# Performance work log

Hardware: AMD Instinct MI355X
Metric: run time of the kernel (lower is better)

## Reference

```python
import jax, jax.numpy as jnp
import numpy as np

B, W, H = 16384, 16, 16
NUM_CLASSES = 1024
EMBED = 4
OUT = 1024

def setup_inputs() -> dict:
    key = jax.random.key(0)
    k0, k1, k2 = jax.random.split(key, 3)
    x = jax.random.randint(k0, (B, W, H), 0, NUM_CLASSES, dtype=jnp.int32)
    W_embed = jax.random.normal(k1, (NUM_CLASSES, EMBED), dtype=jnp.float32) * 0.02
    b_embed = jnp.zeros((EMBED,), dtype=jnp.float32)
    W_dense = jax.random.normal(k2, (EMBED * W * H, OUT), dtype=jnp.float32) * 0.02
    b_dense = jnp.zeros((OUT,), dtype=jnp.float32)
    return {"x": x, "W_embed": W_embed, "b_embed": b_embed, "W_dense": W_dense, "b_dense": b_dense}

def reference(x, W_embed, b_embed, W_dense, b_dense):
    # one_hot(x, C) @ W_embed + b_embed is mathematically a row-gather of W_embed
    emb = W_embed[x] + b_embed                 # (B, W, H, EMBED)
    flat = emb.reshape(emb.shape[0], -1)        # (B, W*H*EMBED)  == rearrange '... w h c -> ... (w h c)'
    return flat @ W_dense + b_dense             # (B, OUT)
```

## Files before the change

kernel.cpp:

```cpp
#include <hip/hip_runtime.h>
#include <stdint.h>
#include <stddef.h>

typedef __attribute__((ext_vector_type(8))) short bf16x8;
typedef __attribute__((ext_vector_type(4))) short bf16x4;
typedef __attribute__((ext_vector_type(4))) float f32x4;

typedef const __attribute__((address_space(1))) void* gptr1_t;
typedef __attribute__((address_space(3))) void* lptr3_t;

#define GLOAD_LDS16(gp, lp) \
  __builtin_amdgcn_global_load_lds((gptr1_t)(gp), (lptr3_t)(lp), 16, 0, 0)

__device__ __forceinline__ uint16_t f2bf(float f) {
  uint32_t u = __builtin_bit_cast(uint32_t, f);
  u += 0x7fffu + ((u >> 16) & 1u);
  return (uint16_t)(u >> 16);
}

#define MB   16384
#define NP   256
#define KDIM 1024
#define NDIM 1024
#define NCLS 1024

#define BM  128
#define BN  256
#define BK  64
#define NK  (KDIM / BK)


__global__ void build_bt_kernel(const float* __restrict__ Wd,
                                uint16_t* __restrict__ Btf) {
  __shared__ uint16_t tile[32][33];
  const int k0 = blockIdx.y * 32;
  const int n0 = blockIdx.x * 32;
  const int tx = threadIdx.x;
  const int ty = threadIdx.y;
  #pragma unroll
  for (int r = 0; r < 32; r += 8)
    tile[ty + r][tx] = f2bf(Wd[(size_t)(k0 + ty + r) * NDIM + n0 + tx]);
  __syncthreads();
  #pragma unroll
  for (int r = 0; r < 32; r += 8) {
    const int n = n0 + ty + r;
    const int k = k0 + tx;
    const int bn = n >> 8, g = (n >> 4) & 15, m = n & 15;
    const int kt = k >> 6, h = (k >> 5) & 1, q = (k >> 3) & 3, e = k & 7;
    Btf[(size_t)((bn * 16 + kt) * 2 + h) * 8192 + (size_t)(g * 64 + q * 16 + m) * 8 + e]
        = tile[tx][ty + r];
  }
}

__global__ __launch_bounds__(512) void fused_gemm_kernel(
    const int* __restrict__ x,
    const float* __restrict__ We,
    const float* __restrict__ be,
    const uint16_t* __restrict__ Btf,
    const float* __restrict__ bias,
    float* __restrict__ C) {
  __shared__ __align__(16) uint16_t web[NCLS * 4];
  __shared__ __align__(16) uint16_t As[2 * 4096];
  __shared__ __align__(16) uint16_t Bs[2 * 8192];

  const int tid  = threadIdx.x;
  const int bm   = blockIdx.x;
  const int bn   = blockIdx.y;
  const int w    = tid >> 6;
  const int l    = tid & 63;
  const int wr   = w >> 2;
  const int wc   = w & 3;
  const int lm   = l & 15;
  const int q4   = l >> 4;

  const int row0 = bm * BM;
  const int col0 = bn * BN;

  {
    const float4 bb = *(const float4*)be;
    #pragma unroll
    for (int c0 = 0; c0 < NCLS; c0 += 512) {
      const int c = c0 + tid;
      const float4 wv = *(const float4*)(We + (size_t)c * 4);
      bf16x4 t;
      t[0] = (short)f2bf(wv.x + bb.x);
      t[1] = (short)f2bf(wv.y + bb.y);
      t[2] = (short)f2bf(wv.z + bb.z);
      t[3] = (short)f2bf(wv.w + bb.w);
      *(bf16x4*)(web + (size_t)c * 4) = t;
    }
  }

  const int mh = w >> 2;
  const int gb = (w & 3) * 2;
  uint16_t* const dA0 = As + (size_t)mh * 4096 + (size_t)((gb    ) * 64 + l) * 8;
  uint16_t* const dA1 = As + (size_t)mh * 4096 + (size_t)((gb + 1) * 64 + l) * 8;
  const int* xr0 = x + (size_t)(row0 + (gb    ) * 16 + lm) * NP + mh * 8 + q4 * 2;
  const int* xr1 = x + (size_t)(row0 + (gb + 1) * 16 + lm) * NP + mh * 8 + q4 * 2;

  f32x4 acc[4][4];
  #pragma unroll
  for (int i = 0; i < 4; i++)
    #pragma unroll
    for (int j = 0; j < 4; j++)
      acc[i][j] = (f32x4){0.f, 0.f, 0.f, 0.f};

  int2 xq0 = *(const int2*)xr0;
  int2 xq1 = *(const int2*)xr1;

  const uint16_t* const btb = Btf + (size_t)bn * (NK * 16384);

  __syncthreads();

  for (int kt = 0; kt < NK; ++kt) {
    const uint16_t* bsrc = btb + (size_t)kt * 16384;
    #pragma unroll
    for (int r = 0; r < 4; ++r)
      GLOAD_LDS16(bsrc + (size_t)r * 4096 + tid * 8, Bs + (size_t)r * 4096 + tid * 8);

    {
      union { bf16x8 v; struct { bf16x4 lo, hi; } s; } u;
      u.s.lo = *(const bf16x4*)(web + ((unsigned)xq0.x * 4u));
      u.s.hi = *(const bf16x4*)(web + ((unsigned)xq0.y * 4u));
      *(bf16x8*)(dA0) = u.v;
      u.s.lo = *(const bf16x4*)(web + ((unsigned)xq1.x * 4u));
      u.s.hi = *(const bf16x4*)(web + ((unsigned)xq1.y * 4u));
      *(bf16x8*)(dA1) = u.v;
    }

    __syncthreads();

    if (kt + 1 < NK) {
      xq0 = *(const int2*)(xr0 + (kt + 1) * 16);
      xq1 = *(const int2*)(xr1 + (kt + 1) * 16);
    }

    #pragma unroll
    for (int h = 0; h < 2; ++h) {
      bf16x8 af[4], bfr[4];
      #pragma unroll
      for (int i = 0; i < 4; i++)
        af[i] = *(const bf16x8*)(As + (size_t)h * 4096 + (size_t)((wr * 4 + i) * 64 + l) * 8);
      #pragma unroll
      for (int j = 0; j < 4; j++)
        bfr[j] = *(const bf16x8*)(Bs + (size_t)h * 8192 + (size_t)((wc * 4 + j) * 64 + l) * 8);

      #pragma unroll
      for (int i = 0; i < 4; i++)
        #pragma unroll
        for (int j = 0; j < 4; j++)
          acc[i][j] = __builtin_amdgcn_mfma_f32_16x16x32_bf16(af[i], bfr[j], acc[i][j], 0, 0, 0);
    }

    __syncthreads();
  }

  float bvals[4];
  #pragma unroll
  for (int j = 0; j < 4; j++)
    bvals[j] = bias[col0 + wc * 64 + j * 16 + lm];

  #pragma unroll
  for (int i = 0; i < 4; i++) {
    const int rbase = row0 + wr * 64 + i * 16 + q4 * 4;
    #pragma unroll
    for (int j = 0; j < 4; j++) {
      const int col = col0 + wc * 64 + j * 16 + lm;
      #pragma unroll
      for (int r = 0; r < 4; r++)
        C[(size_t)(rbase + r) * NDIM + col] = acc[i][j][r] + bvals[j];
    }
  }
}

__global__ void naive_kernel(const int* __restrict__ x,
                             const float* __restrict__ We,
                             const float* __restrict__ be,
                             const float* __restrict__ Wd,
                             const float* __restrict__ bd,
                             float* __restrict__ out) {
  __shared__ float emb[KDIM];
  const int b = blockIdx.x;
  const int tid = threadIdx.x;
  {
    const int cls = x[(size_t)b * NP + tid];
    const float4 e  = *(const float4*)(We + (size_t)cls * 4);
    const float4 bb = *(const float4*)be;
    emb[tid * 4 + 0] = e.x + bb.x;
    emb[tid * 4 + 1] = e.y + bb.y;
    emb[tid * 4 + 2] = e.z + bb.z;
    emb[tid * 4 + 3] = e.w + bb.w;
  }
  __syncthreads();
  float acc0 = bd[tid], acc1 = bd[tid + 256], acc2 = bd[tid + 512], acc3 = bd[tid + 768];
  for (int k = 0; k < KDIM; ++k) {
    const float a = emb[k];
    const float* wv = Wd + (size_t)k * NDIM + tid;
    acc0 += a * wv[0];
    acc1 += a * wv[256];
    acc2 += a * wv[512];
    acc3 += a * wv[768];
  }
  float* o = out + (size_t)b * NDIM + tid;
  o[0] = acc0; o[256] = acc1; o[512] = acc2; o[768] = acc3;
}

extern "C" void kernel_launch(void* const* d_in, const int* in_sizes, int n_in,
                              void* d_out, int out_size, void* d_ws, size_t ws_size,
                              hipStream_t stream) {
  const int*   x  = (const int*)d_in[0];
  const float* We = (const float*)d_in[1];
  const float* be = (const float*)d_in[2];
  const float* Wd = (const float*)d_in[3];
  const float* bd = (const float*)d_in[4];
  float* out = (float*)d_out;

  const size_t needB = (size_t)NDIM * KDIM * sizeof(uint16_t);

  if (ws_size >= needB) {
    uint16_t* Btw = (uint16_t*)d_ws;
    build_bt_kernel<<<dim3(NDIM / 32, KDIM / 32), dim3(32, 8), 0, stream>>>(Wd, Btw);
    fused_gemm_kernel<<<dim3(MB / BM, NDIM / BN), 512, 0, stream>>>(x, We, be, Btw, bd, out);
  } else {
    naive_kernel<<<MB, 256, 0, stream>>>(x, We, be, Wd, bd, out);
  }
}
```

Measured before the change: 123.5 us.

## Software-pipeline GEMM K-loop with double-buffered 32-wide K stages

Restructures the fused embedding-GEMM main loop from 64-wide K tiles with two barriers per tile into 32-wide K stages held in double-buffered LDS. The next stage's B tile (global-to-LDS loads) and gathered A tile are issued while MFMAs run on the current buffer, with a single barrier per stage controlled by explicit vmcnt waits. The B pre-layout in the transpose kernel changes to match, and s_setprio is raised around the MFMA block. The aim is to hide global load latency and cut barrier count, at the cost of finer-grained stages and reliance on hand-placed waitcnt correctness.

```diff
diff --git a/kernel.cpp b/kernel.cpp
--- a/kernel.cpp
+++ b/kernel.cpp
@@ -11,6 +11,9 @@
 
 #define GLOAD_LDS16(gp, lp) \
   __builtin_amdgcn_global_load_lds((gptr1_t)(gp), (lptr3_t)(lp), 16, 0, 0)
+
+#define VMWAIT(N)  asm volatile("s_waitcnt vmcnt(" #N ")" ::: "memory")
+#define MEMFENCE() asm volatile("" ::: "memory")
 
 __device__ __forceinline__ uint16_t f2bf(float f) {
   uint32_t u = __builtin_bit_cast(uint32_t, f);
@@ -26,8 +29,7 @@
 
 #define BM  128
 #define BN  256
-#define BK  64
-#define NK  (KDIM / BK)
+#define NH  32
 
 
 __global__ void build_bt_kernel(const float* __restrict__ Wd,
@@ -46,10 +48,36 @@
     const int n = n0 + ty + r;
     const int k = k0 + tx;
     const int bn = n >> 8, g = (n >> 4) & 15, m = n & 15;
-    const int kt = k >> 6, h = (k >> 5) & 1, q = (k >> 3) & 3, e = k & 7;
-    Btf[(size_t)((bn * 16 + kt) * 2 + h) * 8192 + (size_t)(g * 64 + q * 16 + m) * 8 + e]
+    const int s = k >> 5, q = (k >> 3) & 3, e = k & 7;
+    Btf[(size_t)(bn * NH + s) * 8192 + (size_t)(g * 64 + q * 16 + m) * 8 + e]
         = tile[tx][ty + r];
   }
+}
+
+__device__ __forceinline__ void amat_write(const uint16_t* web, uint16_t* dst, int2 cls) {
+  union { bf16x8 v; struct { bf16x4 lo, hi; } s; } u;
+  u.s.lo = *(const bf16x4*)(web + ((unsigned)cls.x * 4u));
+  u.s.hi = *(const bf16x4*)(web + ((unsigned)cls.y * 4u));
+  *(bf16x8*)dst = u.v;
+}
+
+__device__ __forceinline__ void compute_half(const uint16_t* Asb, const uint16_t* Bsb,
+                                             int wr, int wc, int l, f32x4 acc[4][4]) {
+  bf16x8 af[4], bfr[4];
+  #pragma unroll
+  for (int i = 0; i < 4; i++)
+    af[i] = *(const bf16x8*)(Asb + (size_t)((wr * 4 + i) * 64 + l) * 8);
+  #pragma unroll
+  for (int j = 0; j < 4; j++)
+    bfr[j] = *(const bf16x8*)(Bsb + (size_t)((wc * 4 + j) * 64 + l) * 8);
+
+  __builtin_amdgcn_s_setprio(1);
+  #pragma unroll
+  for (int i = 0; i < 4; i++)
+    #pragma unroll
+    for (int j = 0; j < 4; j++)
+      acc[i][j] = __builtin_amdgcn_mfma_f32_16x16x32_bf16(af[i], bfr[j], acc[i][j], 0, 0, 0);
+  __builtin_amdgcn_s_setprio(0);
 }
 
 __global__ __launch_bounds__(512) void fused_gemm_kernel(
@@ -60,8 +88,8 @@
     const float* __restrict__ bias,
     float* __restrict__ C) {
   __shared__ __align__(16) uint16_t web[NCLS * 4];
-  __shared__ __align__(16) uint16_t As[2 * 4096];
-  __shared__ __align__(16) uint16_t Bs[2 * 8192];
+  __shared__ __align__(16) uint16_t As3[2 * 4096];
+  __shared__ __align__(16) uint16_t Bs3[2 * 8192];
 
   const int tid  = threadIdx.x;
   const int bm   = blockIdx.x;
@@ -91,13 +119,6 @@
     }
   }
 
-  const int mh = w >> 2;
-  const int gb = (w & 3) * 2;
-  uint16_t* const dA0 = As + (size_t)mh * 4096 + (size_t)((gb    ) * 64 + l) * 8;
-  uint16_t* const dA1 = As + (size_t)mh * 4096 + (size_t)((gb + 1) * 64 + l) * 8;
-  const int* xr0 = x + (size_t)(row0 + (gb    ) * 16 + lm) * NP + mh * 8 + q4 * 2;
-  const int* xr1 = x + (size_t)(row0 + (gb + 1) * 16 + lm) * NP + mh * 8 + q4 * 2;
-
   f32x4 acc[4][4];
   #pragma unroll
   for (int i = 0; i < 4; i++)
@@ -105,55 +126,51 @@
     for (int j = 0; j < 4; j++)
       acc[i][j] = (f32x4){0.f, 0.f, 0.f, 0.f};
 
-  int2 xq0 = *(const int2*)xr0;
-  int2 xq1 = *(const int2*)xr1;
-
-  const uint16_t* const btb = Btf + (size_t)bn * (NK * 16384);
-
+  const int* xrow = x + (size_t)(row0 + w * 16 + lm) * NP + q4 * 2;
+  const uint16_t* const btb = Btf + (size_t)bn * (NH * 8192);
+
+  int2 xq0    = *(const int2*)(xrow);
+  int2 xq_next = *(const int2*)(xrow + 8);
   __syncthreads();
 
-  for (int kt = 0; kt < NK; ++kt) {
-    const uint16_t* bsrc = btb + (size_t)kt * 16384;
-    #pragma unroll
-    for (int r = 0; r < 4; ++r)
-      GLOAD_LDS16(bsrc + (size_t)r * 4096 + tid * 8, Bs + (size_t)r * 4096 + tid * 8);
-
-    {
-      union { bf16x8 v; struct { bf16x4 lo, hi; } s; } u;
-      u.s.lo = *(const bf16x4*)(web + ((unsigned)xq0.x * 4u));
-      u.s.hi = *(const bf16x4*)(web + ((unsigned)xq0.y * 4u));
-      *(bf16x8*)(dA0) = u.v;
-      u.s.lo = *(const bf16x4*)(web + ((unsigned)xq1.x * 4u));
-      u.s.hi = *(const bf16x4*)(web + ((unsigned)xq1.y * 4u));
-      *(bf16x8*)(dA1) = u.v;
-    }
-
-    __syncthreads();
-
-    if (kt + 1 < NK) {
-      xq0 = *(const int2*)(xr0 + (kt + 1) * 16);
-      xq1 = *(const int2*)(xr1 + (kt + 1) * 16);
-    }
-
-    #pragma unroll
-    for (int h = 0; h < 2; ++h) {
-      bf16x8 af[4], bfr[4];
-      #pragma unroll
-      for (int i = 0; i < 4; i++)
-        af[i] = *(const bf16x8*)(As + (size_t)h * 4096 + (size_t)((wr * 4 + i) * 64 + l) * 8);
-      #pragma unroll
-      for (int j = 0; j < 4; j++)
-        bfr[j] = *(const bf16x8*)(Bs + (size_t)h * 8192 + (size_t)((wc * 4 + j) * 64 + l) * 8);
-
-      #pragma unroll
-      for (int i = 0; i < 4; i++)
-        #pragma unroll
-        for (int j = 0; j < 4; j++)
-          acc[i][j] = __builtin_amdgcn_mfma_f32_16x16x32_bf16(af[i], bfr[j], acc[i][j], 0, 0, 0);
-    }
-
-    __syncthreads();
-  }
+  GLOAD_LDS16(btb + tid * 8,        Bs3 + tid * 8);
+  GLOAD_LDS16(btb + 4096 + tid * 8, Bs3 + 4096 + tid * 8);
+  amat_write(web, As3 + tid * 8, xq0);
+  asm volatile("s_waitcnt lgkmcnt(0)" ::: "memory");
+
+  for (int s = 0; s < 30; ++s) {
+    const int cb = s & 1, nb = cb ^ 1;
+    int2 xu = xq_next;
+    xq_next = *(const int2*)(xrow + (s + 2) * 8);
+    VMWAIT(1);
+    MEMFENCE();
+    __builtin_amdgcn_s_barrier();
+    MEMFENCE();
+    const uint16_t* bsrc = btb + (size_t)(s + 1) * 8192;
+    GLOAD_LDS16(bsrc + tid * 8,        Bs3 + (size_t)nb * 8192 + tid * 8);
+    GLOAD_LDS16(bsrc + 4096 + tid * 8, Bs3 + (size_t)nb * 8192 + 4096 + tid * 8);
+    amat_write(web, As3 + (size_t)nb * 4096 + tid * 8, xu);
+    compute_half(As3 + (size_t)cb * 4096, Bs3 + (size_t)cb * 8192, wr, wc, l, acc);
+  }
+
+  {
+    int2 xu = xq_next;
+    VMWAIT(0);
+    MEMFENCE();
+    __builtin_amdgcn_s_barrier();
+    MEMFENCE();
+    const uint16_t* bsrc = btb + (size_t)31 * 8192;
+    GLOAD_LDS16(bsrc + tid * 8,        Bs3 + 8192 + tid * 8);
+    GLOAD_LDS16(bsrc + 4096 + tid * 8, Bs3 + 8192 + 4096 + tid * 8);
+    amat_write(web, As3 + 4096 + tid * 8, xu);
+    compute_half(As3, Bs3, wr, wc, l, acc);
+  }
+
+  VMWAIT(0);
+  MEMFENCE();
+  __builtin_amdgcn_s_barrier();
+  MEMFENCE();
+  compute_half(As3 + 4096, Bs3 + 8192, wr, wc, l, acc);
 
   float bvals[4];
   #pragma unroll
```

Measured after the change: 119.7 us (median of 2 runs). 3.1% less time.

## Load B fragments directly into registers and drop LDS staging and barriers

Applied to the files above, without the earlier changes.

The GEMM now keeps B fragments in registers, loaded straight from global memory with a one-step register prefetch, and builds A fragments directly from the LDS embedding table. This removes the As/Bs LDS tiles and the per-iteration __syncthreads. The tile shrinks to 64x256 with 256 threads, so each wave owns 64 columns across all 64 rows, and the MFMA blocks are wrapped in s_setprio. The cost is that B is reloaded from global/L2 by every block with no LDS sharing between waves, and there are twice as many blocks, which raises total B traffic.

```diff
diff --git a/kernel.cpp b/kernel.cpp
--- a/kernel.cpp
+++ b/kernel.cpp
@@ -5,12 +5,6 @@
 typedef __attribute__((ext_vector_type(8))) short bf16x8;
 typedef __attribute__((ext_vector_type(4))) short bf16x4;
 typedef __attribute__((ext_vector_type(4))) float f32x4;
-
-typedef const __attribute__((address_space(1))) void* gptr1_t;
-typedef __attribute__((address_space(3))) void* lptr3_t;
-
-#define GLOAD_LDS16(gp, lp) \
-  __builtin_amdgcn_global_load_lds((gptr1_t)(gp), (lptr3_t)(lp), 16, 0, 0)
 
 __device__ __forceinline__ uint16_t f2bf(float f) {
   uint32_t u = __builtin_bit_cast(uint32_t, f);
@@ -24,10 +18,7 @@
 #define NDIM 1024
 #define NCLS 1024
 
-#define BM  128
-#define BN  256
-#define BK  64
-#define NK  (KDIM / BK)
+#define NH  32
 
 
 __global__ void build_bt_kernel(const float* __restrict__ Wd,
@@ -46,13 +37,13 @@
     const int n = n0 + ty + r;
     const int k = k0 + tx;
     const int bn = n >> 8, g = (n >> 4) & 15, m = n & 15;
-    const int kt = k >> 6, h = (k >> 5) & 1, q = (k >> 3) & 3, e = k & 7;
-    Btf[(size_t)((bn * 16 + kt) * 2 + h) * 8192 + (size_t)(g * 64 + q * 16 + m) * 8 + e]
+    const int s = k >> 5, q = (k >> 3) & 3, e = k & 7;
+    Btf[(size_t)(bn * NH + s) * 8192 + (size_t)(g * 64 + q * 16 + m) * 8 + e]
         = tile[tx][ty + r];
   }
 }
 
-__global__ __launch_bounds__(512) void fused_gemm_kernel(
+__global__ __launch_bounds__(256) void fused_gemm_kernel(
     const int* __restrict__ x,
     const float* __restrict__ We,
     const float* __restrict__ be,
@@ -60,26 +51,22 @@
     const float* __restrict__ bias,
     float* __restrict__ C) {
   __shared__ __align__(16) uint16_t web[NCLS * 4];
-  __shared__ __align__(16) uint16_t As[2 * 4096];
-  __shared__ __align__(16) uint16_t Bs[2 * 8192];
-
-  const int tid  = threadIdx.x;
-  const int bm   = blockIdx.x;
-  const int bn   = blockIdx.y;
-  const int w    = tid >> 6;
-  const int l    = tid & 63;
-  const int wr   = w >> 2;
-  const int wc   = w & 3;
-  const int lm   = l & 15;
-  const int q4   = l >> 4;
-
-  const int row0 = bm * BM;
-  const int col0 = bn * BN;
+
+  const int tid = threadIdx.x;
+  const int bm  = blockIdx.x;
+  const int bn  = blockIdx.y;
+  const int w   = tid >> 6;
+  const int l   = tid & 63;
+  const int lm  = l & 15;
+  const int q4  = l >> 4;
+
+  const int row0 = bm * 64;
+  const int col0 = bn * 256;
 
   {
     const float4 bb = *(const float4*)be;
     #pragma unroll
-    for (int c0 = 0; c0 < NCLS; c0 += 512) {
+    for (int c0 = 0; c0 < NCLS; c0 += 256) {
       const int c = c0 + tid;
       const float4 wv = *(const float4*)(We + (size_t)c * 4);
       bf16x4 t;
@@ -90,13 +77,13 @@
       *(bf16x4*)(web + (size_t)c * 4) = t;
     }
   }
-
-  const int mh = w >> 2;
-  const int gb = (w & 3) * 2;
-  uint16_t* const dA0 = As + (size_t)mh * 4096 + (size_t)((gb    ) * 64 + l) * 8;
-  uint16_t* const dA1 = As + (size_t)mh * 4096 + (size_t)((gb + 1) * 64 + l) * 8;
-  const int* xr0 = x + (size_t)(row0 + (gb    ) * 16 + lm) * NP + mh * 8 + q4 * 2;
-  const int* xr1 = x + (size_t)(row0 + (gb + 1) * 16 + lm) * NP + mh * 8 + q4 * 2;
+  __syncthreads();
+
+  const int* xr0 = x + (size_t)(row0 +  0 + lm) * NP + q4 * 2;
+  const int* xr1 = x + (size_t)(row0 + 16 + lm) * NP + q4 * 2;
+  const int* xr2 = x + (size_t)(row0 + 32 + lm) * NP + q4 * 2;
+  const int* xr3 = x + (size_t)(row0 + 48 + lm) * NP + q4 * 2;
+  const uint16_t* bp = Btf + (size_t)bn * (NH * 8192) + (size_t)((w * 4) * 64 + l) * 8;
 
   f32x4 acc[4][4];
   #pragma unroll
@@ -105,67 +92,78 @@
     for (int j = 0; j < 4; j++)
       acc[i][j] = (f32x4){0.f, 0.f, 0.f, 0.f};
 
-  int2 xq0 = *(const int2*)xr0;
-  int2 xq1 = *(const int2*)xr1;
-
-  const uint16_t* const btb = Btf + (size_t)bn * (NK * 16384);
-
-  __syncthreads();
-
-  for (int kt = 0; kt < NK; ++kt) {
-    const uint16_t* bsrc = btb + (size_t)kt * 16384;
-    #pragma unroll
-    for (int r = 0; r < 4; ++r)
-      GLOAD_LDS16(bsrc + (size_t)r * 4096 + tid * 8, Bs + (size_t)r * 4096 + tid * 8);
-
-    {
-      union { bf16x8 v; struct { bf16x4 lo, hi; } s; } u;
-      u.s.lo = *(const bf16x4*)(web + ((unsigned)xq0.x * 4u));
-      u.s.hi = *(const bf16x4*)(web + ((unsigned)xq0.y * 4u));
-      *(bf16x8*)(dA0) = u.v;
-      u.s.lo = *(const bf16x4*)(web + ((unsigned)xq1.x * 4u));
-      u.s.hi = *(const bf16x4*)(web + ((unsigned)xq1.y * 4u));
-      *(bf16x8*)(dA1) = u.v;
-    }
-
-    __syncthreads();
-
-    if (kt + 1 < NK) {
-      xq0 = *(const int2*)(xr0 + (kt + 1) * 16);
-      xq1 = *(const int2*)(xr1 + (kt + 1) * 16);
-    }
-
-    #pragma unroll
-    for (int h = 0; h < 2; ++h) {
-      bf16x8 af[4], bfr[4];
-      #pragma unroll
-      for (int i = 0; i < 4; i++)
-        af[i] = *(const bf16x8*)(As + (size_t)h * 4096 + (size_t)((wr * 4 + i) * 64 + l) * 8);
+  int2 xq[4], xn[4];
+  bf16x8 bcur[4], bnxt[4];
+  xq[0] = *(const int2*)xr0;
+  xq[1] = *(const int2*)xr1;
+  xq[2] = *(const int2*)xr2;
+  xq[3] = *(const int2*)xr3;
+  #pragma unroll
+  for (int j = 0; j < 4; j++)
+    bcur[j] = *(const bf16x8*)(bp + (size_t)j * 512);
+
+  for (int s = 0; s < NH - 1; ++s) {
+    const uint16_t* bq = bp + (size_t)(s + 1) * 8192;
+    #pragma unroll
+    for (int j = 0; j < 4; j++)
+      bnxt[j] = *(const bf16x8*)(bq + (size_t)j * 512);
+    xn[0] = *(const int2*)(xr0 + (s + 1) * 8);
+    xn[1] = *(const int2*)(xr1 + (s + 1) * 8);
+    xn[2] = *(const int2*)(xr2 + (s + 1) * 8);
+    xn[3] = *(const int2*)(xr3 + (s + 1) * 8);
+
+    bf16x8 af[4];
+    #pragma unroll
+    for (int i = 0; i < 4; i++) {
+      union { bf16x8 v; struct { bf16x4 lo, hi; } s_; } u;
+      u.s_.lo = *(const bf16x4*)(web + ((unsigned)xq[i].x * 4u));
+      u.s_.hi = *(const bf16x4*)(web + ((unsigned)xq[i].y * 4u));
+      af[i] = u.v;
+    }
+
+    __builtin_amdgcn_s_setprio(1);
+    #pragma unroll
+    for (int i = 0; i < 4; i++)
       #pragma unroll
       for (int j = 0; j < 4; j++)
-        bfr[j] = *(const bf16x8*)(Bs + (size_t)h * 8192 + (size_t)((wc * 4 + j) * 64 + l) * 8);
-
+        acc[i][j] = __builtin_amdgcn_mfma_f32_16x16x32_bf16(af[i], bcur[j], acc[i][j], 0, 0, 0);
+    __builtin_amdgcn_s_setprio(0);
+
+    #pragma unroll
+    for (int j = 0; j < 4; j++) bcur[j] = bnxt[j];
+    #pragma unroll
+    for (int i = 0; i < 4; i++) xq[i] = xn[i];
+  }
+
+  {
+    bf16x8 af[4];
+    #pragma unroll
+    for (int i = 0; i < 4; i++) {
+      union { bf16x8 v; struct { bf16x4 lo, hi; } s_; } u;
+      u.s_.lo = *(const bf16x4*)(web + ((unsigned)xq[i].x * 4u));
+      u.s_.hi = *(const bf16x4*)(web + ((unsigned)xq[i].y * 4u));
+      af[i] = u.v;
+    }
+    __builtin_amdgcn_s_setprio(1);
+    #pragma unroll
+    for (int i = 0; i < 4; i++)
       #pragma unroll
-      for (int i = 0; i < 4; i++)
-        #pragma unroll
-        for (int j = 0; j < 4; j++)
-          acc[i][j] = __builtin_amdgcn_mfma_f32_16x16x32_bf16(af[i], bfr[j], acc[i][j], 0, 0, 0);
-    }
-
-    __syncthreads();
+      for (int j = 0; j < 4; j++)
+        acc[i][j] = __builtin_amdgcn_mfma_f32_16x16x32_bf16(af[i], bcur[j], acc[i][j], 0, 0, 0);
+    __builtin_amdgcn_s_setprio(0);
   }
 
   float bvals[4];
   #pragma unroll
   for (int j = 0; j < 4; j++)
-    bvals[j] = bias[col0 + wc * 64 + j * 16 + lm];
+    bvals[j] = bias[col0 + w * 64 + j * 16 + lm];
 
   #pragma unroll
   for (int i = 0; i < 4; i++) {
-    const int rbase = row0 + wr * 64 + i * 16 + q4 * 4;
+    const int rbase = row0 + i * 16 + q4 * 4;
     #pragma unroll
     for (int j = 0; j < 4; j++) {
-      const int col = col0 + wc * 64 + j * 16 + lm;
+      const int col = col0 + w * 64 + j * 16 + lm;
       #pragma unroll
       for (int r = 0; r < 4; r++)
         C[(size_t)(rbase + r) * NDIM + col] = acc[i][j][r] + bvals[j];
@@ -220,7 +218,7 @@
   if (ws_size >= needB) {
     uint16_t* Btw = (uint16_t*)d_ws;
     build_bt_kernel<<<dim3(NDIM / 32, KDIM / 32), dim3(32, 8), 0, stream>>>(Wd, Btw);
-    fused_gemm_kernel<<<dim3(MB / BM, NDIM / BN), 512, 0, stream>>>(x, We, be, Btw, bd, out);
+    fused_gemm_kernel<<<dim3(MB / 64, NDIM / 256), 256, 0, stream>>>(x, We, be, Btw, bd, out);
   } else {
     naive_kernel<<<MB, 256, 0, stream>>>(x, We, be, Wd, bd, out);
   }
```

Result: slower. 175.8 us (+42.3%).
